# Optimization experiments

Measured on AMD Instinct MI355X. Metric: run time of the kernel, lower is better.

Reference implementation:

```python
import jax, jax.numpy as jnp
import numpy as np

N_FFT = 256
HOP = 64
HS = 126  # window hop in STFT frames (hard-coded in original)


def _stft(x):
    # torch.stft(center=True, pad_mode='reflect', window=None -> rectangular,
    # onesided=True, normalized=False). x: [B, N] -> [B, T, F] (time-major,
    # matching the module's permute(0,1,3,2)).
    pad = N_FFT // 2
    xp = jnp.pad(x, ((0, 0), (pad, pad)), mode='reflect')
    T = x.shape[-1] // HOP + 1
    idx = jnp.arange(T)[:, None] * HOP + jnp.arange(N_FFT)[None, :]  # [T, n_fft]
    frames = xp[:, idx]  # [B, T, n_fft]
    return jnp.fft.rfft(frames, axis=-1)  # [B, T, F=129]


def _spec_match(mix, aux):
    mixS = _stft(mix[:, 0, :])  # [B, Tm, F] complex
    auxS = _stft(aux[:, 0, :])  # [B, Ta, F] complex
    B, Tm, F = mixS.shape
    Ta = auxS.shape[1]
    length = (Ta - Tm) // HS
    pad = HS - (Ta - Tm) % HS
    auxS = jnp.pad(auxS, ((0, 0), (0, pad), (0, 0)))
    # All sliding windows at once: [B, W, Tm, F]
    W = length + 2
    widx = jnp.arange(W)[:, None] * HS + jnp.arange(Tm)[None, :]  # [W, Tm]
    wins = auxS[:, widx, :]  # [B, W, Tm, F]
    # Real part of complex cosine similarity, elementwise
    m = mixS[:, None]  # [B, 1, Tm, F]
    sim = (m.real * wins.real + m.imag * wins.imag) / (jnp.abs(m) * jnp.abs(wins))
    flat = sim.reshape(B, W, -1)
    n = flat.shape[-1]
    # torch.median = lower median; torch.median returns NaN if any NaN present
    srt = jnp.sort(flat, axis=-1)
    med = srt[..., (n - 1) // 2]
    med = jnp.where(jnp.isnan(flat).any(-1), -jnp.inf, med)
    best = jnp.argmax(med, axis=1)  # [B], first max like Python max()
    sel = jnp.take_along_axis(wins, best[:, None, None, None], axis=1)  # [B,1,Tm,F]
    return jnp.concatenate([sel.real, sel.imag], axis=1)  # [B, 2, Tm, F]


def setup_inputs() -> dict:
    key = jax.random.key(0)
    k1, k2 = jax.random.split(key)
    mix = jax.random.normal(k1, (8, 1, 65536), dtype=jnp.float32)
    aux = jax.random.normal(k2, (8, 1, 262144), dtype=jnp.float32)
    return {"mix": mix, "aux": aux}


def reference(mix, aux):
    return _spec_match(mix, aux)
```

## Files before the change

kernel.cpp:

```cpp
#include <hip/hip_runtime.h>
#include <math.h>

constexpr int NFFT  = 256;
constexpr int HOP   = 64;
constexpr int NBIN  = 129;
constexpr int NB    = 8;
constexpr int LMIX  = 65536;
constexpr int LAUX  = 262144;
constexpr int TM    = 1025;
constexpr int TA    = 4097;
constexpr int TROWS = 4175;
constexpr int HS    = 126;
constexpr int W     = 26;
constexpr int NJOBS = NB * W;
constexpr int NVAL  = TM * NBIN;
constexpr int KMED  = (NVAL - 1) / 2;
constexpr int CHUNKS = 8;
constexpr int NBA   = 1024;
constexpr int FPB   = 4;
constexpr int MIXBLKS = (TM + FPB - 1) / FPB;
constexpr int AUXBLKS = (TROWS + FPB - 1) / FPB;

constexpr size_t MIXN_OFF  = 0;
constexpr size_t MIXN_BYTES = (size_t)NB * TM * NBIN * sizeof(float2);
constexpr size_t AUXN_OFF  = MIXN_OFF + MIXN_BYTES;
constexpr size_t AUXN_BYTES = (size_t)NB * TROWS * NBIN * sizeof(float2);
constexpr size_t HIST_OFF  = AUXN_OFF + AUXN_BYTES;
constexpr size_t HIST_BYTES = (size_t)NJOBS * CHUNKS * NBA * 4;
constexpr size_t CAND_OFF  = HIST_OFF + HIST_BYTES;
constexpr size_t CAND_BYTES = (size_t)NJOBS * NVAL * 4;
constexpr size_t NAN_OFF   = CAND_OFF + CAND_BYTES;
constexpr size_t NAN_BYTES = (size_t)NJOBS * CHUNKS * 4;
constexpr size_t NCAND_OFF = NAN_OFF + NAN_BYTES;
constexpr size_t KREM_OFF  = NCAND_OFF + 832;
constexpr size_t MED_OFF   = KREM_OFF + 832;

__device__ __forceinline__ float2 twiddle(int k) {
    float s, c;
    sincosf((float)(-2.0 * 3.14159265358979323846 / 256.0) * (float)k, &s, &c);
    return make_float2(c, s);
}

__global__ void stft_all(const float* __restrict__ mix, const float* __restrict__ aux,
                         float2* __restrict__ mixN, float2* __restrict__ auxN,
                         unsigned* __restrict__ ncand)
{
    constexpr int NX = 64 * (FPB - 1) + NFFT;
    __shared__ float  xs[NX];
    __shared__ float2 Y[FPB][16][16];
    __shared__ float2 cis16[16];

    const int tid = threadIdx.x;
    const int b   = blockIdx.y;
    const int bx  = blockIdx.x;
    const bool isMix = bx < MIXBLKS;
    const int f0 = (isMix ? bx : bx - MIXBLKS) * FPB;
    const int L       = isMix ? LMIX : LAUX;
    const int Tframes = isMix ? TM : TA;
    const int Trows   = isMix ? TM : TROWS;
    const float* x    = isMix ? mix : aux;
    float2* out       = isMix ? mixN : auxN;

    if (bx == 0 && b == 0 && tid < NJOBS) ncand[tid] = 0u;

    if (tid < 16) cis16[tid] = twiddle(16 * tid);

    for (int i = tid; i < NX; i += 256) {
        int j = f0 * HOP + i - 128;
        if (j < 0) j = -j;
        if (j >= L) j = 2 * L - 2 - j;
        xs[i] = x[(size_t)b * L + j];
    }
    __syncthreads();

    const int n1 = (tid >> 4) & 15;
    const int r  = tid & 15;
    #pragma unroll
    for (int f = 0; f < FPB; ++f) {
        float re = 0.f, im = 0.f;
        int idx = 0;
        #pragma unroll
        for (int n2 = 0; n2 < 16; ++n2) {
            float  v = xs[f * HOP + n1 + 16 * n2];
            float2 t = cis16[idx];
            re = fmaf(v, t.x, re);
            im = fmaf(v, t.y, im);
            idx = (idx + r) & 15;
        }
        Y[f][n1][r] = make_float2(re, im);
    }
    __syncthreads();

    const float QNAN = __int_as_float(0x7FC00000);
    auto emit = [&](int fr, int k, float ar, float ai) {
        if (fr >= Trows) return;
        float2 o;
        if (fr < Tframes) {
            float inv = rsqrtf(ar * ar + ai * ai);
            o = make_float2(ar * inv, ai * inv);
        } else {
            o = make_float2(QNAN, QNAN);
        }
        out[((size_t)b * Trows + fr) * NBIN + k] = o;
    };

    {
        const int jjA = tid, jjB = tid + 256;
        const int fA = jjA / NBIN, kA = jjA - fA * NBIN;
        const int fB = jjB / NBIN, kB = jjB - fB * NBIN;
        const float2 dkA = twiddle(kA);
        const float2 dkB = twiddle(kB);
        float trA = 1.f, tiA = 0.f, arA = 0.f, aiA = 0.f;
        float trB = 1.f, tiB = 0.f, arB = 0.f, aiB = 0.f;
        #pragma unroll
        for (int s = 0; s < 16; ++s) {
            float2 yA = Y[fA][s][kA & 15];
            float2 yB = Y[fB][s][kB & 15];
            arA = fmaf(trA, yA.x, arA); arA = fmaf(-tiA, yA.y, arA);
            aiA = fmaf(trA, yA.y, aiA); aiA = fmaf( tiA, yA.x, aiA);
            arB = fmaf(trB, yB.x, arB); arB = fmaf(-tiB, yB.y, arB);
            aiB = fmaf(trB, yB.y, aiB); aiB = fmaf( tiB, yB.x, aiB);
            float nrA = trA * dkA.x - tiA * dkA.y;
            tiA = fmaf(trA, dkA.y, tiA * dkA.x); trA = nrA;
            float nrB = trB * dkB.x - tiB * dkB.y;
            tiB = fmaf(trB, dkB.y, tiB * dkB.x); trB = nrB;
        }
        emit(f0 + fA, kA, arA, aiA);
        emit(f0 + fB, kB, arB, aiB);
    }
    if (tid < FPB * NBIN - 512) {
        const int jj = 512 + tid;
        const int f = jj / NBIN, k = jj - f * NBIN;
        const float2 dk = twiddle(k);
        float tr = 1.f, ti = 0.f, ar = 0.f, ai = 0.f;
        #pragma unroll
        for (int s = 0; s < 16; ++s) {
            float2 y = Y[f][s][k & 15];
            ar = fmaf(tr, y.x, ar); ar = fmaf(-ti, y.y, ar);
            ai = fmaf(tr, y.y, ai); ai = fmaf( ti, y.x, ai);
            float nr = tr * dk.x - ti * dk.y;
            ti = fmaf(tr, dk.y, ti * dk.x); tr = nr;
        }
        emit(f0 + f, k, ar, ai);
    }
}

__device__ __forceinline__ unsigned flip_key(float s) {
    unsigned u = __float_as_uint(s);
    return (u & 0x80000000u) ? ~u : (u | 0x80000000u);
}

__device__ __forceinline__ unsigned qbin(float s) {
    if (!(s == s)) return (unsigned)(NBA - 1);
    int bq = (int)floorf(fmaf(s, 512.f, 512.f));
    bq = max(0, min(NBA - 1, bq));
    return (unsigned)bq;
}

template<int PER>
__device__ __forceinline__ void rank_find(const unsigned (&bins)[PER], unsigned target,
                                          unsigned& out_bin, unsigned& out_rem)
{
    __shared__ unsigned wtot[4];
    __shared__ unsigned result[2];
    const int tid  = threadIdx.x;
    const int lane = tid & 63;
    const int wid  = tid >> 6;

    unsigned st = 0;
    #pragma unroll
    for (int i = 0; i < PER; ++i) st += bins[i];

    unsigned inc = st;
    #pragma unroll
    for (int d = 1; d < 64; d <<= 1) {
        unsigned v = __shfl_up(inc, d);
        if (lane >= d) inc += v;
    }
    if (lane == 63) wtot[wid] = inc;
    __syncthreads();

    unsigned wbase = 0;
    for (int wme = 0; wme < wid; ++wme) wbase += wtot[wme];
    unsigned ex = wbase + inc - st;
    if ((ex <= target) && (target < ex + st)) {
        unsigned cum = ex;
        #pragma unroll
        for (int i = 0; i < PER; ++i) {
            if (cum + bins[i] > target) {
                result[0] = (unsigned)(tid * PER + i);
                result[1] = target - cum;
                break;
            }
            cum += bins[i];
        }
    }
    __syncthreads();
    out_bin = result[0];
    out_rem = result[1];
}

__global__ void sim_hist(const float2* __restrict__ mixN, const float2* __restrict__ auxN,
                         unsigned* __restrict__ hist, unsigned* __restrict__ nanCnt)
{
    constexpr int NCOPY   = 4;
    constexpr int HSTRIDE = NBA + 1;
    __shared__ unsigned lh[NCOPY * HSTRIDE];
    __shared__ unsigned bnan;
    const int tid   = threadIdx.x;
    const int chunk = blockIdx.x;
    const int job   = blockIdx.y;
    const int b = job / W;
    const int w = job - b * W;
    unsigned* lhc = lh + ((tid >> 4) & (NCOPY - 1)) * HSTRIDE;

    for (int i = tid; i < NCOPY * HSTRIDE; i += 256) lh[i] = 0;
    if (tid == 0) bnan = 0;
    __syncthreads();

    unsigned localnan = 0;
    const float2* mrow = mixN + (size_t)b * TM * NBIN;
    const float2* arow = auxN + ((size_t)b * TROWS + (size_t)w * HS) * NBIN;

    const int pad = b & 1;
    const int lim = pad + ((NVAL - pad) & ~1);

    for (int i = pad + (chunk * 256 + tid) * 2; i < lim; i += CHUNKS * 512) {
        float4 mv = *reinterpret_cast<const float4*>(mrow + i);
        float4 av = *reinterpret_cast<const float4*>(arow + i);
        float s0 = fmaf(mv.x, av.x, mv.y * av.y);
        float s1 = fmaf(mv.z, av.z, mv.w * av.w);
        if (!(s0 == s0)) localnan++;
        if (!(s1 == s1)) localnan++;
        atomicAdd(&lhc[qbin(s0)], 1u);
        atomicAdd(&lhc[qbin(s1)], 1u);
    }
    if (chunk == 0 && tid == 0) {
        int ie = pad ? 0 : NVAL - 1;
        float2 m = mrow[ie];
        float2 a = arow[ie];
        float s = fmaf(m.x, a.x, m.y * a.y);
        if (!(s == s)) localnan++;
        atomicAdd(&lhc[qbin(s)], 1u);
    }
    if (localnan) atomicAdd(&bnan, localnan);
    __syncthreads();

    unsigned* gh = hist + ((size_t)job * CHUNKS + chunk) * NBA;
    for (int i = tid; i < NBA; i += 256)
        gh[i] = lh[i] + lh[HSTRIDE + i] + lh[2 * HSTRIDE + i] + lh[3 * HSTRIDE + i];
    if (tid == 0) nanCnt[job * CHUNKS + chunk] = bnan;
}

__global__ void sim_compact(const float2* __restrict__ mixN, const float2* __restrict__ auxN,
                            const unsigned* __restrict__ hist, unsigned* __restrict__ cand,
                            unsigned* __restrict__ ncand, unsigned* __restrict__ krem)
{
    const int tid   = threadIdx.x;
    const int chunk = blockIdx.x;
    const int job   = blockIdx.y;
    const int b = job / W;
    const int w = job - b * W;

    unsigned bins[NBA / 256];
    const unsigned* h = hist + (size_t)job * CHUNKS * NBA;
    #pragma unroll
    for (int i = 0; i < NBA / 256; ++i) {
        unsigned v = 0;
        int bin = tid * (NBA / 256) + i;
        #pragma unroll
        for (int c = 0; c < CHUNKS; ++c) v += h[(size_t)c * NBA + bin];
        bins[i] = v;
    }
    unsigned sb, rem;
    rank_find<NBA / 256>(bins, (unsigned)KMED, sb, rem);
    if (chunk == 0 && tid == 0) krem[job] = rem;

    unsigned* candj  = cand + (size_t)job * NVAL;
    unsigned* ncandj = ncand + job;
    const int lane = tid & 63;

    const float2* mrow = mixN + (size_t)b * TM * NBIN;
    const float2* arow = auxN + ((size_t)b * TROWS + (size_t)w * HS) * NBIN;

    const int pad = b & 1;
    const int lim = pad + ((NVAL - pad) & ~1);

    for (int i = pad + (chunk * 256 + tid) * 2; i < lim; i += CHUNKS * 512) {
        float4 mv = *reinterpret_cast<const float4*>(mrow + i);
        float4 av = *reinterpret_cast<const float4*>(arow + i);
        float sv[2];
        sv[0] = fmaf(mv.x, av.x, mv.y * av.y);
        sv[1] = fmaf(mv.z, av.z, mv.w * av.w);
        #pragma unroll
        for (int u = 0; u < 2; ++u) {
            bool pred = (qbin(sv[u]) == sb);
            unsigned long long m = __ballot(pred);
            if (m) {
                int leader = __ffsll(m) - 1;
                unsigned base = 0;
                if (lane == leader) base = atomicAdd(ncandj, (unsigned)__popcll(m));
                base = (unsigned)__shfl((int)base, leader);
                if (pred) candj[base + __popcll(m & ((1ull << lane) - 1ull))] = flip_key(sv[u]);
            }
        }
    }
    if (chunk == 0 && tid == 0) {
        int ie = pad ? 0 : NVAL - 1;
        float2 m = mrow[ie];
        float2 a = arow[ie];
        float s = fmaf(m.x, a.x, m.y * a.y);
        if (qbin(s) == sb) {
            unsigned idx = atomicAdd(ncandj, 1u);
            candj[idx] = flip_key(s);
        }
    }
}

__global__ void select_kernel(const unsigned* __restrict__ cand, const unsigned* __restrict__ ncand,
                              const unsigned* __restrict__ krem, const unsigned* __restrict__ nanCnt,
                              float* __restrict__ med)
{
    __shared__ unsigned h[2048];
    const int job = blockIdx.x;
    const int tid = threadIdx.x;
    const unsigned* c = cand + (size_t)job * NVAL;
    const unsigned n = ncand[job];
    unsigned pref = 0, tgt = krem[job];

    for (int ph = 0; ph < 3; ++ph) {
        for (int i = tid; i < 2048; i += 256) h[i] = 0;
        __syncthreads();
        for (unsigned i = tid; i < n; i += 256) {
            unsigned k = c[i];
            if (ph == 0) atomicAdd(&h[k >> 21], 1u);
            else if (ph == 1) { if ((k >> 21) == (pref >> 21)) atomicAdd(&h[(k >> 10) & 2047u], 1u); }
            else { if ((k >> 10) == (pref >> 10)) atomicAdd(&h[k & 1023u], 1u); }
        }
        __syncthreads();

        unsigned bins[8];
        #pragma unroll
        for (int i = 0; i < 8; ++i) bins[i] = h[tid * 8 + i];
        unsigned sb, rem;
        rank_find<8>(bins, tgt, sb, rem);

        if (ph == 0)      pref = sb << 21;
        else if (ph == 1) pref |= sb << 10;
        else              pref |= sb;
        tgt = rem;
        __syncthreads();
    }

    if (tid == 0) {
        unsigned nan = 0;
        #pragma unroll
        for (int c2 = 0; c2 < CHUNKS; ++c2) nan += nanCnt[job * CHUNKS + c2];
        unsigned key = pref;
        unsigned u = (key & 0x80000000u) ? (key ^ 0x80000000u) : ~key;
        med[job] = (nan > 0u) ? -INFINITY : __uint_as_float(u);
    }
}

__global__ void gather_stft(const float* __restrict__ x, const float* __restrict__ med,
                            float* __restrict__ out)
{
    constexpr int NX = 64 * (FPB - 1) + NFFT;
    __shared__ float  xs[NX];
    __shared__ float2 Y[FPB][16][16];
    __shared__ float2 cis16[16];
    __shared__ int sh_best;

    const int tid = threadIdx.x;
    const int b   = blockIdx.y;
    const int t0  = blockIdx.x * FPB;

    if (tid == 0) {
        float mx = -INFINITY; int bi = 0;
        for (int w = 0; w < W; ++w) {
            float v = med[b * W + w];
            if (v > mx) { mx = v; bi = w; }
        }
        sh_best = bi;
    }
    if (tid < 16) cis16[tid] = twiddle(16 * tid);
    __syncthreads();

    const int fr0 = sh_best * HS + t0;

    for (int i = tid; i < NX; i += 256) {
        int j = fr0 * HOP + i - 128;
        if (j < 0) j = -j;
        if (j >= LAUX) j = 2 * LAUX - 2 - j;
        j = max(0, min(LAUX - 1, j));
        xs[i] = x[(size_t)b * LAUX + j];
    }
    __syncthreads();

    const int n1 = (tid >> 4) & 15;
    const int r  = tid & 15;
    #pragma unroll
    for (int f = 0; f < FPB; ++f) {
        float re = 0.f, im = 0.f;
        int idx = 0;
        #pragma unroll
        for (int n2 = 0; n2 < 16; ++n2) {
            float  v = xs[f * HOP + n1 + 16 * n2];
            float2 t = cis16[idx];
            re = fmaf(v, t.x, re);
            im = fmaf(v, t.y, im);
            idx = (idx + r) & 15;
        }
        Y[f][n1][r] = make_float2(re, im);
    }
    __syncthreads();

    for (int jj = tid; jj < FPB * NBIN; jj += 256) {
        int f  = jj / NBIN;
        int k  = jj - f * NBIN;
        int t  = t0 + f;
        if (t >= TM) continue;
        float ar = 0.f, ai = 0.f;
        if (fr0 + f < TA) {
            float2 dk = twiddle(k);
            float tr = 1.f, ti = 0.f;
            #pragma unroll
            for (int s = 0; s < 16; ++s) {
                float2 y = Y[f][s][k & 15];
                ar = fmaf(tr, y.x, ar); ar = fmaf(-ti, y.y, ar);
                ai = fmaf(tr, y.y, ai); ai = fmaf( ti, y.x, ai);
                float nr = tr * dk.x - ti * dk.y;
                ti = fmaf(tr, dk.y, ti * dk.x);
                tr = nr;
            }
        }
        size_t o = (size_t)t * NBIN + k;
        out[(size_t)(b * 2 + 0) * NVAL + o] = ar;
        out[(size_t)(b * 2 + 1) * NVAL + o] = ai;
    }
}

extern "C" void kernel_launch(void* const* d_in, const int* in_sizes, int n_in,
                              void* d_out, int out_size, void* d_ws, size_t ws_size,
                              hipStream_t stream)
{
    const float* mix = (const float*)d_in[0];
    const float* aux = (const float*)d_in[1];
    float* out = (float*)d_out;
    char* ws = (char*)d_ws;

    float2*   mixN = (float2*)(ws + MIXN_OFF);
    float2*   auxN = (float2*)(ws + AUXN_OFF);
    unsigned* hist = (unsigned*)(ws + HIST_OFF);
    unsigned* cand = (unsigned*)(ws + CAND_OFF);
    unsigned* nanC = (unsigned*)(ws + NAN_OFF);
    unsigned* ncand= (unsigned*)(ws + NCAND_OFF);
    unsigned* krem = (unsigned*)(ws + KREM_OFF);
    float*    med  = (float*)(ws + MED_OFF);

    stft_all<<<dim3(MIXBLKS + AUXBLKS, NB), 256, 0, stream>>>(mix, aux, mixN, auxN, ncand);
    sim_hist<<<dim3(CHUNKS, NJOBS), 256, 0, stream>>>(mixN, auxN, hist, nanC);
    sim_compact<<<dim3(CHUNKS, NJOBS), 256, 0, stream>>>(mixN, auxN, hist, cand, ncand, krem);
    select_kernel<<<NJOBS, 256, 0, stream>>>(cand, ncand, krem, nanC, med);
    gather_stft<<<dim3((TM + FPB - 1) / FPB, NB), 256, 0, stream>>>(aux, med, out);
}
```

Before: 136.5 us.

## Materialize similarity keys once and replace recompute-compaction with in-shared candidate select

The similarity pass now writes every flipped-float key to a workspace buffer while building the histogram. A small scan kernel then picks the median bin, and the select kernel compacts matching keys from that buffer into shared memory before the radix refinement. This replaces the second read of mixN/auxN with its global atomic compaction. The STFT kernels also use a 256-entry shared twiddle table in place of recursive twiddle multiplication, and loop over frames inside the n2 loop. The cost is writing and re-reading about 110 MB of keys, and a fallback full scan if a bin holds more than SEL_CAP entries.

```diff
diff --git a/kernel.cpp b/kernel.cpp
--- a/kernel.cpp
+++ b/kernel.cpp
@@ -14,41 +14,36 @@
 constexpr int W     = 26;
 constexpr int NJOBS = NB * W;
 constexpr int NVAL  = TM * NBIN;
+constexpr int NVALP = 132228;
 constexpr int KMED  = (NVAL - 1) / 2;
 constexpr int CHUNKS = 8;
 constexpr int NBA   = 1024;
 constexpr int FPB   = 4;
 constexpr int MIXBLKS = (TM + FPB - 1) / FPB;
 constexpr int AUXBLKS = (TROWS + FPB - 1) / FPB;
+constexpr int SEL_CAP = 12288;
 
 constexpr size_t MIXN_OFF  = 0;
 constexpr size_t MIXN_BYTES = (size_t)NB * TM * NBIN * sizeof(float2);
 constexpr size_t AUXN_OFF  = MIXN_OFF + MIXN_BYTES;
 constexpr size_t AUXN_BYTES = (size_t)NB * TROWS * NBIN * sizeof(float2);
-constexpr size_t HIST_OFF  = AUXN_OFF + AUXN_BYTES;
+constexpr size_t KEYS_OFF  = AUXN_OFF + AUXN_BYTES;
+constexpr size_t KEYS_BYTES = (size_t)NJOBS * NVALP * 4;
+constexpr size_t HIST_OFF  = KEYS_OFF + KEYS_BYTES;
 constexpr size_t HIST_BYTES = (size_t)NJOBS * CHUNKS * NBA * 4;
-constexpr size_t CAND_OFF  = HIST_OFF + HIST_BYTES;
-constexpr size_t CAND_BYTES = (size_t)NJOBS * NVAL * 4;
-constexpr size_t NAN_OFF   = CAND_OFF + CAND_BYTES;
+constexpr size_t NAN_OFF   = HIST_OFF + HIST_BYTES;
 constexpr size_t NAN_BYTES = (size_t)NJOBS * CHUNKS * 4;
-constexpr size_t NCAND_OFF = NAN_OFF + NAN_BYTES;
-constexpr size_t KREM_OFF  = NCAND_OFF + 832;
+constexpr size_t SELBIN_OFF= NAN_OFF + NAN_BYTES;
+constexpr size_t KREM_OFF  = SELBIN_OFF + 832;
 constexpr size_t MED_OFF   = KREM_OFF + 832;
 
-__device__ __forceinline__ float2 twiddle(int k) {
-    float s, c;
-    sincosf((float)(-2.0 * 3.14159265358979323846 / 256.0) * (float)k, &s, &c);
-    return make_float2(c, s);
-}
-
 __global__ void stft_all(const float* __restrict__ mix, const float* __restrict__ aux,
-                         float2* __restrict__ mixN, float2* __restrict__ auxN,
-                         unsigned* __restrict__ ncand)
+                         float2* __restrict__ mixN, float2* __restrict__ auxN)
 {
     constexpr int NX = 64 * (FPB - 1) + NFFT;
     __shared__ float  xs[NX];
-    __shared__ float2 Y[FPB][16][16];
-    __shared__ float2 cis16[16];
+    __shared__ float2 Yl[FPB][16][16];
+    __shared__ float2 tw[256];
 
     const int tid = threadIdx.x;
     const int b   = blockIdx.y;
@@ -61,9 +56,8 @@
     const float* x    = isMix ? mix : aux;
     float2* out       = isMix ? mixN : auxN;
 
-    if (bx == 0 && b == 0 && tid < NJOBS) ncand[tid] = 0u;
-
-    if (tid < 16) cis16[tid] = twiddle(16 * tid);
+    { float sv, cv; sincosf((float)(-2.0 * 3.14159265358979323846 / 256.0) * (float)tid, &sv, &cv);
+      tw[tid] = make_float2(cv, sv); }
 
     for (int i = tid; i < NX; i += 256) {
         int j = f0 * HOP + i - 128;
@@ -75,20 +69,26 @@
 
     const int n1 = (tid >> 4) & 15;
     const int r  = tid & 15;
-    #pragma unroll
-    for (int f = 0; f < FPB; ++f) {
-        float re = 0.f, im = 0.f;
+    float reA[FPB], imA[FPB];
+    #pragma unroll
+    for (int f = 0; f < FPB; ++f) { reA[f] = 0.f; imA[f] = 0.f; }
+    {
         int idx = 0;
+        const int step = (r * 16) & 255;
         #pragma unroll
         for (int n2 = 0; n2 < 16; ++n2) {
-            float  v = xs[f * HOP + n1 + 16 * n2];
-            float2 t = cis16[idx];
-            re = fmaf(v, t.x, re);
-            im = fmaf(v, t.y, im);
-            idx = (idx + r) & 15;
-        }
-        Y[f][n1][r] = make_float2(re, im);
-    }
+            float2 t = tw[idx];
+            #pragma unroll
+            for (int f = 0; f < FPB; ++f) {
+                float v = xs[f * HOP + n1 + 16 * n2];
+                reA[f] = fmaf(v, t.x, reA[f]);
+                imA[f] = fmaf(v, t.y, imA[f]);
+            }
+            idx = (idx + step) & 255;
+        }
+    }
+    #pragma unroll
+    for (int f = 0; f < FPB; ++f) Yl[f][n1][r] = make_float2(reA[f], imA[f]);
     __syncthreads();
 
     const float QNAN = __int_as_float(0x7FC00000);
@@ -108,22 +108,17 @@
         const int jjA = tid, jjB = tid + 256;
         const int fA = jjA / NBIN, kA = jjA - fA * NBIN;
         const int fB = jjB / NBIN, kB = jjB - fB * NBIN;
-        const float2 dkA = twiddle(kA);
-        const float2 dkB = twiddle(kB);
-        float trA = 1.f, tiA = 0.f, arA = 0.f, aiA = 0.f;
-        float trB = 1.f, tiB = 0.f, arB = 0.f, aiB = 0.f;
+        float arA = 0.f, aiA = 0.f, arB = 0.f, aiB = 0.f;
+        int ia = 0, ib = 0;
         #pragma unroll
         for (int s = 0; s < 16; ++s) {
-            float2 yA = Y[fA][s][kA & 15];
-            float2 yB = Y[fB][s][kB & 15];
-            arA = fmaf(trA, yA.x, arA); arA = fmaf(-tiA, yA.y, arA);
-            aiA = fmaf(trA, yA.y, aiA); aiA = fmaf( tiA, yA.x, aiA);
-            arB = fmaf(trB, yB.x, arB); arB = fmaf(-tiB, yB.y, arB);
-            aiB = fmaf(trB, yB.y, aiB); aiB = fmaf( tiB, yB.x, aiB);
-            float nrA = trA * dkA.x - tiA * dkA.y;
-            tiA = fmaf(trA, dkA.y, tiA * dkA.x); trA = nrA;
-            float nrB = trB * dkB.x - tiB * dkB.y;
-            tiB = fmaf(trB, dkB.y, tiB * dkB.x); trB = nrB;
+            float2 tA = tw[ia], tB = tw[ib];
+            float2 yA = Yl[fA][s][kA & 15], yB = Yl[fB][s][kB & 15];
+            arA = fmaf(tA.x, yA.x, arA); arA = fmaf(-tA.y, yA.y, arA);
+            aiA = fmaf(tA.x, yA.y, aiA); aiA = fmaf( tA.y, yA.x, aiA);
+            arB = fmaf(tB.x, yB.x, arB); arB = fmaf(-tB.y, yB.y, arB);
+            aiB = fmaf(tB.x, yB.y, aiB); aiB = fmaf( tB.y, yB.x, aiB);
+            ia = (ia + kA) & 255; ib = (ib + kB) & 255;
         }
         emit(f0 + fA, kA, arA, aiA);
         emit(f0 + fB, kB, arB, aiB);
@@ -131,15 +126,15 @@
     if (tid < FPB * NBIN - 512) {
         const int jj = 512 + tid;
         const int f = jj / NBIN, k = jj - f * NBIN;
-        const float2 dk = twiddle(k);
-        float tr = 1.f, ti = 0.f, ar = 0.f, ai = 0.f;
+        float ar = 0.f, ai = 0.f;
+        int ia = 0;
         #pragma unroll
         for (int s = 0; s < 16; ++s) {
-            float2 y = Y[f][s][k & 15];
-            ar = fmaf(tr, y.x, ar); ar = fmaf(-ti, y.y, ar);
-            ai = fmaf(tr, y.y, ai); ai = fmaf( ti, y.x, ai);
-            float nr = tr * dk.x - ti * dk.y;
-            ti = fmaf(tr, dk.y, ti * dk.x); tr = nr;
+            float2 t = tw[ia];
+            float2 y = Yl[f][s][k & 15];
+            ar = fmaf(t.x, y.x, ar); ar = fmaf(-t.y, y.y, ar);
+            ai = fmaf(t.x, y.y, ai); ai = fmaf( t.y, y.x, ai);
+            ia = (ia + k) & 255;
         }
         emit(f0 + f, k, ar, ai);
     }
@@ -149,7 +144,10 @@
     unsigned u = __float_as_uint(s);
     return (u & 0x80000000u) ? ~u : (u | 0x80000000u);
 }
-
+__device__ __forceinline__ float unflip_key(unsigned k) {
+    unsigned u = (k & 0x80000000u) ? (k ^ 0x80000000u) : ~k;
+    return __uint_as_float(u);
+}
 __device__ __forceinline__ unsigned qbin(float s) {
     if (!(s == s)) return (unsigned)(NBA - 1);
     int bq = (int)floorf(fmaf(s, 512.f, 512.f));
@@ -200,8 +198,9 @@
     out_rem = result[1];
 }
 
-__global__ void sim_hist(const float2* __restrict__ mixN, const float2* __restrict__ auxN,
-                         unsigned* __restrict__ hist, unsigned* __restrict__ nanCnt)
+__global__ void sim_keys(const float2* __restrict__ mixN, const float2* __restrict__ auxN,
+                         unsigned* __restrict__ keys, unsigned* __restrict__ hist,
+                         unsigned* __restrict__ nanCnt)
 {
     constexpr int NCOPY   = 4;
     constexpr int HSTRIDE = NBA + 1;
@@ -221,6 +220,7 @@
     unsigned localnan = 0;
     const float2* mrow = mixN + (size_t)b * TM * NBIN;
     const float2* arow = auxN + ((size_t)b * TROWS + (size_t)w * HS) * NBIN;
+    unsigned* kj = keys + (size_t)job * NVALP;
 
     const int pad = b & 1;
     const int lim = pad + ((NVAL - pad) & ~1);
@@ -234,6 +234,7 @@
         if (!(s1 == s1)) localnan++;
         atomicAdd(&lhc[qbin(s0)], 1u);
         atomicAdd(&lhc[qbin(s1)], 1u);
+        *reinterpret_cast<uint2*>(kj + i) = make_uint2(flip_key(s0), flip_key(s1));
     }
     if (chunk == 0 && tid == 0) {
         int ie = pad ? 0 : NVAL - 1;
@@ -242,6 +243,7 @@
         float s = fmaf(m.x, a.x, m.y * a.y);
         if (!(s == s)) localnan++;
         atomicAdd(&lhc[qbin(s)], 1u);
+        kj[ie] = flip_key(s);
     }
     if (localnan) atomicAdd(&bnan, localnan);
     __syncthreads();
@@ -252,102 +254,99 @@
     if (tid == 0) nanCnt[job * CHUNKS + chunk] = bnan;
 }
 
-__global__ void sim_compact(const float2* __restrict__ mixN, const float2* __restrict__ auxN,
-                            const unsigned* __restrict__ hist, unsigned* __restrict__ cand,
-                            unsigned* __restrict__ ncand, unsigned* __restrict__ krem)
-{
-    const int tid   = threadIdx.x;
-    const int chunk = blockIdx.x;
-    const int job   = blockIdx.y;
-    const int b = job / W;
-    const int w = job - b * W;
-
-    unsigned bins[NBA / 256];
+__global__ void scan_bins(const unsigned* __restrict__ hist, unsigned* __restrict__ selbin,
+                          unsigned* __restrict__ krem)
+{
+    constexpr int PER = NBA / 256;
+    const int tid = threadIdx.x;
+    const int job = blockIdx.x;
     const unsigned* h = hist + (size_t)job * CHUNKS * NBA;
-    #pragma unroll
-    for (int i = 0; i < NBA / 256; ++i) {
+
+    unsigned bins[PER];
+    #pragma unroll
+    for (int i = 0; i < PER; ++i) {
         unsigned v = 0;
-        int bin = tid * (NBA / 256) + i;
+        int bin = tid * PER + i;
         #pragma unroll
         for (int c = 0; c < CHUNKS; ++c) v += h[(size_t)c * NBA + bin];
         bins[i] = v;
     }
     unsigned sb, rem;
-    rank_find<NBA / 256>(bins, (unsigned)KMED, sb, rem);
-    if (chunk == 0 && tid == 0) krem[job] = rem;
-
-    unsigned* candj  = cand + (size_t)job * NVAL;
-    unsigned* ncandj = ncand + job;
-    const int lane = tid & 63;
-
-    const float2* mrow = mixN + (size_t)b * TM * NBIN;
-    const float2* arow = auxN + ((size_t)b * TROWS + (size_t)w * HS) * NBIN;
-
-    const int pad = b & 1;
-    const int lim = pad + ((NVAL - pad) & ~1);
-
-    for (int i = pad + (chunk * 256 + tid) * 2; i < lim; i += CHUNKS * 512) {
-        float4 mv = *reinterpret_cast<const float4*>(mrow + i);
-        float4 av = *reinterpret_cast<const float4*>(arow + i);
-        float sv[2];
-        sv[0] = fmaf(mv.x, av.x, mv.y * av.y);
-        sv[1] = fmaf(mv.z, av.z, mv.w * av.w);
-        #pragma unroll
-        for (int u = 0; u < 2; ++u) {
-            bool pred = (qbin(sv[u]) == sb);
-            unsigned long long m = __ballot(pred);
-            if (m) {
-                int leader = __ffsll(m) - 1;
-                unsigned base = 0;
-                if (lane == leader) base = atomicAdd(ncandj, (unsigned)__popcll(m));
-                base = (unsigned)__shfl((int)base, leader);
-                if (pred) candj[base + __popcll(m & ((1ull << lane) - 1ull))] = flip_key(sv[u]);
-            }
-        }
-    }
-    if (chunk == 0 && tid == 0) {
-        int ie = pad ? 0 : NVAL - 1;
-        float2 m = mrow[ie];
-        float2 a = arow[ie];
-        float s = fmaf(m.x, a.x, m.y * a.y);
-        if (qbin(s) == sb) {
-            unsigned idx = atomicAdd(ncandj, 1u);
-            candj[idx] = flip_key(s);
-        }
-    }
-}
-
-__global__ void select_kernel(const unsigned* __restrict__ cand, const unsigned* __restrict__ ncand,
+    rank_find<PER>(bins, (unsigned)KMED, sb, rem);
+    if (tid == 0) { selbin[job] = sb; krem[job] = rem; }
+}
+
+__global__ void select_kernel(const unsigned* __restrict__ keys, const unsigned* __restrict__ selbin,
                               const unsigned* __restrict__ krem, const unsigned* __restrict__ nanCnt,
                               float* __restrict__ med)
 {
+    __shared__ unsigned ck[SEL_CAP];
     __shared__ unsigned h[2048];
+    __shared__ unsigned nov;
     const int job = blockIdx.x;
     const int tid = threadIdx.x;
-    const unsigned* c = cand + (size_t)job * NVAL;
-    const unsigned n = ncand[job];
+    const unsigned* kj = keys + (size_t)job * NVALP;
+    const unsigned sb = selbin[job];
+
+    if (tid == 0) nov = 0;
+    __syncthreads();
+
+    const uint4* k4 = reinterpret_cast<const uint4*>(kj);
+    const int n4 = NVAL / 4;
+    for (int i = tid; i < n4; i += 256) {
+        uint4 v = k4[i];
+        unsigned kk[4] = { v.x, v.y, v.z, v.w };
+        #pragma unroll
+        for (int u = 0; u < 4; ++u) {
+            if (qbin(unflip_key(kk[u])) == sb) {
+                unsigned p = atomicAdd(&nov, 1u);
+                if (p < SEL_CAP) ck[p] = kk[u];
+            }
+        }
+    }
+    if (tid == 0) {
+        unsigned kk = kj[NVAL - 1];
+        if (qbin(unflip_key(kk)) == sb) {
+            unsigned p = atomicAdd(&nov, 1u);
+            if (p < SEL_CAP) ck[p] = kk;
+        }
+    }
+    __syncthreads();
+
+    const unsigned n = nov;
+    const bool fits = (n <= (unsigned)SEL_CAP);
     unsigned pref = 0, tgt = krem[job];
 
     for (int ph = 0; ph < 3; ++ph) {
         for (int i = tid; i < 2048; i += 256) h[i] = 0;
         __syncthreads();
-        for (unsigned i = tid; i < n; i += 256) {
-            unsigned k = c[i];
-            if (ph == 0) atomicAdd(&h[k >> 21], 1u);
-            else if (ph == 1) { if ((k >> 21) == (pref >> 21)) atomicAdd(&h[(k >> 10) & 2047u], 1u); }
-            else { if ((k >> 10) == (pref >> 10)) atomicAdd(&h[k & 1023u], 1u); }
+        if (fits) {
+            for (unsigned i = tid; i < n; i += 256) {
+                unsigned k = ck[i];
+                if (ph == 0) atomicAdd(&h[k >> 21], 1u);
+                else if (ph == 1) { if ((k >> 21) == (pref >> 21)) atomicAdd(&h[(k >> 10) & 2047u], 1u); }
+                else { if ((k >> 10) == (pref >> 10)) atomicAdd(&h[k & 1023u], 1u); }
+            }
+        } else {
+            for (int i = tid; i < NVAL; i += 256) {
+                unsigned k = kj[i];
+                if (qbin(unflip_key(k)) != sb) continue;
+                if (ph == 0) atomicAdd(&h[k >> 21], 1u);
+                else if (ph == 1) { if ((k >> 21) == (pref >> 21)) atomicAdd(&h[(k >> 10) & 2047u], 1u); }
+                else { if ((k >> 10) == (pref >> 10)) atomicAdd(&h[k & 1023u], 1u); }
+            }
         }
         __syncthreads();
 
         unsigned bins[8];
         #pragma unroll
         for (int i = 0; i < 8; ++i) bins[i] = h[tid * 8 + i];
-        unsigned sb, rem;
-        rank_find<8>(bins, tgt, sb, rem);
-
-        if (ph == 0)      pref = sb << 21;
-        else if (ph == 1) pref |= sb << 10;
-        else              pref |= sb;
+        unsigned sb2, rem;
+        rank_find<8>(bins, tgt, sb2, rem);
+
+        if (ph == 0)      pref = sb2 << 21;
+        else if (ph == 1) pref |= sb2 << 10;
+        else              pref |= sb2;
         tgt = rem;
         __syncthreads();
     }
@@ -355,10 +354,8 @@
     if (tid == 0) {
         unsigned nan = 0;
         #pragma unroll
-        for (int c2 = 0; c2 < CHUNKS; ++c2) nan += nanCnt[job * CHUNKS + c2];
-        unsigned key = pref;
-        unsigned u = (key & 0x80000000u) ? (key ^ 0x80000000u) : ~key;
-        med[job] = (nan > 0u) ? -INFINITY : __uint_as_float(u);
+        for (int c = 0; c < CHUNKS; ++c) nan += nanCnt[job * CHUNKS + c];
+        med[job] = (nan > 0u) ? -INFINITY : unflip_key(pref);
     }
 }
 
@@ -367,8 +364,8 @@
 {
     constexpr int NX = 64 * (FPB - 1) + NFFT;
     __shared__ float  xs[NX];
-    __shared__ float2 Y[FPB][16][16];
-    __shared__ float2 cis16[16];
+    __shared__ float2 Yl[FPB][16][16];
+    __shared__ float2 tw[256];
     __shared__ int sh_best;
 
     const int tid = threadIdx.x;
@@ -383,7 +380,8 @@
         }
         sh_best = bi;
     }
-    if (tid < 16) cis16[tid] = twiddle(16 * tid);
+    { float sv, cv; sincosf((float)(-2.0 * 3.14159265358979323846 / 256.0) * (float)tid, &sv, &cv);
+      tw[tid] = make_float2(cv, sv); }
     __syncthreads();
 
     const int fr0 = sh_best * HS + t0;
@@ -399,20 +397,26 @@
 
     const int n1 = (tid >> 4) & 15;
     const int r  = tid & 15;
-    #pragma unroll
-    for (int f = 0; f < FPB; ++f) {
-        float re = 0.f, im = 0.f;
+    float reA[FPB], imA[FPB];
+    #pragma unroll
+    for (int f = 0; f < FPB; ++f) { reA[f] = 0.f; imA[f] = 0.f; }
+    {
         int idx = 0;
+        const int step = (r * 16) & 255;
         #pragma unroll
         for (int n2 = 0; n2 < 16; ++n2) {
-            float  v = xs[f * HOP + n1 + 16 * n2];
-            float2 t = cis16[idx];
-            re = fmaf(v, t.x, re);
-            im = fmaf(v, t.y, im);
-            idx = (idx + r) & 15;
-        }
-        Y[f][n1][r] = make_float2(re, im);
-    }
+            float2 t = tw[idx];
+            #pragma unroll
+            for (int f = 0; f < FPB; ++f) {
+                float v = xs[f * HOP + n1 + 16 * n2];
+                reA[f] = fmaf(v, t.x, reA[f]);
+                imA[f] = fmaf(v, t.y, imA[f]);
+            }
+            idx = (idx + step) & 255;
+        }
+    }
+    #pragma unroll
+    for (int f = 0; f < FPB; ++f) Yl[f][n1][r] = make_float2(reA[f], imA[f]);
     __syncthreads();
 
     for (int jj = tid; jj < FPB * NBIN; jj += 256) {
@@ -422,16 +426,14 @@
         if (t >= TM) continue;
         float ar = 0.f, ai = 0.f;
         if (fr0 + f < TA) {
-            float2 dk = twiddle(k);
-            float tr = 1.f, ti = 0.f;
+            int ia = 0;
             #pragma unroll
             for (int s = 0; s < 16; ++s) {
-                float2 y = Y[f][s][k & 15];
-                ar = fmaf(tr, y.x, ar); ar = fmaf(-ti, y.y, ar);
-                ai = fmaf(tr, y.y, ai); ai = fmaf( ti, y.x, ai);
-                float nr = tr * dk.x - ti * dk.y;
-                ti = fmaf(tr, dk.y, ti * dk.x);
-                tr = nr;
+                float2 tv = tw[ia];
+                float2 y = Yl[f][s][k & 15];
+                ar = fmaf(tv.x, y.x, ar); ar = fmaf(-tv.y, y.y, ar);
+                ai = fmaf(tv.x, y.y, ai); ai = fmaf( tv.y, y.x, ai);
+                ia = (ia + k) & 255;
             }
         }
         size_t o = (size_t)t * NBIN + k;
@@ -451,16 +453,16 @@
 
     float2*   mixN = (float2*)(ws + MIXN_OFF);
     float2*   auxN = (float2*)(ws + AUXN_OFF);
+    unsigned* keys = (unsigned*)(ws + KEYS_OFF);
     unsigned* hist = (unsigned*)(ws + HIST_OFF);
-    unsigned* cand = (unsigned*)(ws + CAND_OFF);
     unsigned* nanC = (unsigned*)(ws + NAN_OFF);
-    unsigned* ncand= (unsigned*)(ws + NCAND_OFF);
+    unsigned* selb = (unsigned*)(ws + SELBIN_OFF);
     unsigned* krem = (unsigned*)(ws + KREM_OFF);
     float*    med  = (float*)(ws + MED_OFF);
 
-    stft_all<<<dim3(MIXBLKS + AUXBLKS, NB), 256, 0, stream>>>(mix, aux, mixN, auxN, ncand);
-    sim_hist<<<dim3(CHUNKS, NJOBS), 256, 0, stream>>>(mixN, auxN, hist, nanC);
-    sim_compact<<<dim3(CHUNKS, NJOBS), 256, 0, stream>>>(mixN, auxN, hist, cand, ncand, krem);
-    select_kernel<<<NJOBS, 256, 0, stream>>>(cand, ncand, krem, nanC, med);
-    gather_stft<<<dim3((TM + FPB - 1) / FPB, NB), 256, 0, stream>>>(aux, med, out);
-}
+    stft_all<<<dim3(MIXBLKS + AUXBLKS, NB), 256, 0, stream>>>(mix, aux, mixN, auxN);
+    sim_keys<<<dim3(CHUNKS, NJOBS), 256, 0, stream>>>(mixN, auxN, keys, hist, nanC);
+    scan_bins<<<NJOBS, 256, 0, stream>>>(hist, selb, krem);
+    select_kernel<<<NJOBS, 256, 0, stream>>>(keys, selb, krem, nanC, med);
+    gather_stft<<<dim3(MIXBLKS, NB), 256, 0, stream>>>(aux, med, out);
+}
```

Result: slower. 195.1 us (+43.0%).

## Swizzle workgroup IDs across batches and widen STFT frames per block

Applied to the files above, without the earlier changes.

Flattens every grid to 1D and decodes the block index so that the batch index is the fastest-varying component. The likely aim is to spread consecutive workgroups over XCDs and memory channels. The STFT kernel now handles 8 frames per block instead of 4, with the first-stage DFT loop interchanged so each twiddle load serves all frames. Per-bin twiddles come from a shared 256-entry table rather than sincosf in each thread. Larger blocks mean fewer workgroups and more registers per thread, which may reduce occupancy.

```diff
diff --git a/kernel.cpp b/kernel.cpp
--- a/kernel.cpp
+++ b/kernel.cpp
@@ -17,9 +17,11 @@
 constexpr int KMED  = (NVAL - 1) / 2;
 constexpr int CHUNKS = 8;
 constexpr int NBA   = 1024;
-constexpr int FPB   = 4;
+constexpr int FPB   = 8;
 constexpr int MIXBLKS = (TM + FPB - 1) / FPB;
 constexpr int AUXBLKS = (TROWS + FPB - 1) / FPB;
+constexpr int GFPB  = 4;
+constexpr int GBLKS = (TM + GFPB - 1) / GFPB;
 
 constexpr size_t MIXN_OFF  = 0;
 constexpr size_t MIXN_BYTES = (size_t)NB * TM * NBIN * sizeof(float2);
@@ -35,9 +37,11 @@
 constexpr size_t KREM_OFF  = NCAND_OFF + 832;
 constexpr size_t MED_OFF   = KREM_OFF + 832;
 
+constexpr float TWOPI_N = (float)(-2.0 * 3.14159265358979323846 / 256.0);
+
 __device__ __forceinline__ float2 twiddle(int k) {
     float s, c;
-    sincosf((float)(-2.0 * 3.14159265358979323846 / 256.0) * (float)k, &s, &c);
+    sincosf(TWOPI_N * (float)k, &s, &c);
     return make_float2(c, s);
 }
 
@@ -47,22 +51,25 @@
 {
     constexpr int NX = 64 * (FPB - 1) + NFFT;
     __shared__ float  xs[NX];
-    __shared__ float2 Y[FPB][16][16];
+    __shared__ float2 Yl[FPB][16][16];
+    __shared__ float2 tw256[256];
     __shared__ float2 cis16[16];
 
-    const int tid = threadIdx.x;
-    const int b   = blockIdx.y;
-    const int bx  = blockIdx.x;
-    const bool isMix = bx < MIXBLKS;
-    const int f0 = (isMix ? bx : bx - MIXBLKS) * FPB;
+    const int tid  = threadIdx.x;
+    const int wgid = blockIdx.x;
+    const int b    = wgid & 7;
+    const int t    = wgid >> 3;
+    const bool isMix = t < MIXBLKS;
+    const int f0 = (isMix ? t : t - MIXBLKS) * FPB;
     const int L       = isMix ? LMIX : LAUX;
     const int Tframes = isMix ? TM : TA;
     const int Trows   = isMix ? TM : TROWS;
     const float* x    = isMix ? mix : aux;
     float2* out       = isMix ? mixN : auxN;
 
-    if (bx == 0 && b == 0 && tid < NJOBS) ncand[tid] = 0u;
-
+    if (wgid == 0 && tid < NJOBS) ncand[tid] = 0u;
+
+    tw256[tid] = twiddle(tid);
     if (tid < 16) cis16[tid] = twiddle(16 * tid);
 
     for (int i = tid; i < NX; i += 256) {
@@ -75,19 +82,24 @@
 
     const int n1 = (tid >> 4) & 15;
     const int r  = tid & 15;
-    #pragma unroll
-    for (int f = 0; f < FPB; ++f) {
-        float re = 0.f, im = 0.f;
+    {
+        float reA[FPB], imA[FPB];
+        #pragma unroll
+        for (int f = 0; f < FPB; ++f) { reA[f] = 0.f; imA[f] = 0.f; }
         int idx = 0;
         #pragma unroll
         for (int n2 = 0; n2 < 16; ++n2) {
-            float  v = xs[f * HOP + n1 + 16 * n2];
-            float2 t = cis16[idx];
-            re = fmaf(v, t.x, re);
-            im = fmaf(v, t.y, im);
+            float2 tv = cis16[idx];
+            #pragma unroll
+            for (int f = 0; f < FPB; ++f) {
+                float v = xs[f * HOP + n1 + 16 * n2];
+                reA[f] = fmaf(v, tv.x, reA[f]);
+                imA[f] = fmaf(v, tv.y, imA[f]);
+            }
             idx = (idx + r) & 15;
         }
-        Y[f][n1][r] = make_float2(re, im);
+        #pragma unroll
+        for (int f = 0; f < FPB; ++f) Yl[f][n1][r] = make_float2(reA[f], imA[f]);
     }
     __syncthreads();
 
@@ -105,37 +117,39 @@
     };
 
     {
-        const int jjA = tid, jjB = tid + 256;
-        const int fA = jjA / NBIN, kA = jjA - fA * NBIN;
-        const int fB = jjB / NBIN, kB = jjB - fB * NBIN;
-        const float2 dkA = twiddle(kA);
-        const float2 dkB = twiddle(kB);
-        float trA = 1.f, tiA = 0.f, arA = 0.f, aiA = 0.f;
-        float trB = 1.f, tiB = 0.f, arB = 0.f, aiB = 0.f;
+        int fc[4], kc[4];
+        float tr[4], ti[4], ar[4], ai[4];
+        float2 dk[4];
+        #pragma unroll
+        for (int c = 0; c < 4; ++c) {
+            int jj = tid + 256 * c;
+            fc[c] = jj / NBIN; kc[c] = jj - fc[c] * NBIN;
+            dk[c] = tw256[kc[c]];
+            tr[c] = 1.f; ti[c] = 0.f; ar[c] = 0.f; ai[c] = 0.f;
+        }
         #pragma unroll
         for (int s = 0; s < 16; ++s) {
-            float2 yA = Y[fA][s][kA & 15];
-            float2 yB = Y[fB][s][kB & 15];
-            arA = fmaf(trA, yA.x, arA); arA = fmaf(-tiA, yA.y, arA);
-            aiA = fmaf(trA, yA.y, aiA); aiA = fmaf( tiA, yA.x, aiA);
-            arB = fmaf(trB, yB.x, arB); arB = fmaf(-tiB, yB.y, arB);
-            aiB = fmaf(trB, yB.y, aiB); aiB = fmaf( tiB, yB.x, aiB);
-            float nrA = trA * dkA.x - tiA * dkA.y;
-            tiA = fmaf(trA, dkA.y, tiA * dkA.x); trA = nrA;
-            float nrB = trB * dkB.x - tiB * dkB.y;
-            tiB = fmaf(trB, dkB.y, tiB * dkB.x); trB = nrB;
-        }
-        emit(f0 + fA, kA, arA, aiA);
-        emit(f0 + fB, kB, arB, aiB);
-    }
-    if (tid < FPB * NBIN - 512) {
-        const int jj = 512 + tid;
+            #pragma unroll
+            for (int c = 0; c < 4; ++c) {
+                float2 y = Yl[fc[c]][s][kc[c] & 15];
+                ar[c] = fmaf(tr[c], y.x, ar[c]); ar[c] = fmaf(-ti[c], y.y, ar[c]);
+                ai[c] = fmaf(tr[c], y.y, ai[c]); ai[c] = fmaf( ti[c], y.x, ai[c]);
+                float nr = tr[c] * dk[c].x - ti[c] * dk[c].y;
+                ti[c] = fmaf(tr[c], dk[c].y, ti[c] * dk[c].x);
+                tr[c] = nr;
+            }
+        }
+        #pragma unroll
+        for (int c = 0; c < 4; ++c) emit(f0 + fc[c], kc[c], ar[c], ai[c]);
+    }
+    if (tid < FPB * NBIN - 1024) {
+        const int jj = 1024 + tid;
         const int f = jj / NBIN, k = jj - f * NBIN;
-        const float2 dk = twiddle(k);
+        const float2 dk = tw256[k];
         float tr = 1.f, ti = 0.f, ar = 0.f, ai = 0.f;
         #pragma unroll
         for (int s = 0; s < 16; ++s) {
-            float2 y = Y[f][s][k & 15];
+            float2 y = Yl[f][s][k & 15];
             ar = fmaf(tr, y.x, ar); ar = fmaf(-ti, y.y, ar);
             ai = fmaf(tr, y.y, ai); ai = fmaf( ti, y.x, ai);
             float nr = tr * dk.x - ti * dk.y;
@@ -149,7 +163,6 @@
     unsigned u = __float_as_uint(s);
     return (u & 0x80000000u) ? ~u : (u | 0x80000000u);
 }
-
 __device__ __forceinline__ unsigned qbin(float s) {
     if (!(s == s)) return (unsigned)(NBA - 1);
     int bq = (int)floorf(fmaf(s, 512.f, 512.f));
@@ -208,10 +221,12 @@
     __shared__ unsigned lh[NCOPY * HSTRIDE];
     __shared__ unsigned bnan;
     const int tid   = threadIdx.x;
-    const int chunk = blockIdx.x;
-    const int job   = blockIdx.y;
-    const int b = job / W;
-    const int w = job - b * W;
+    const int wgid  = blockIdx.x;
+    const int b     = wgid & 7;
+    const int rest  = wgid >> 3;
+    const int w     = rest / CHUNKS;
+    const int chunk = rest - w * CHUNKS;
+    const int job   = b * W + w;
     unsigned* lhc = lh + ((tid >> 4) & (NCOPY - 1)) * HSTRIDE;
 
     for (int i = tid; i < NCOPY * HSTRIDE; i += 256) lh[i] = 0;
@@ -257,10 +272,12 @@
                             unsigned* __restrict__ ncand, unsigned* __restrict__ krem)
 {
     const int tid   = threadIdx.x;
-    const int chunk = blockIdx.x;
-    const int job   = blockIdx.y;
-    const int b = job / W;
-    const int w = job - b * W;
+    const int wgid  = blockIdx.x;
+    const int b     = wgid & 7;
+    const int rest  = wgid >> 3;
+    const int w     = rest / CHUNKS;
+    const int chunk = rest - w * CHUNKS;
+    const int job   = b * W + w;
 
     unsigned bins[NBA / 256];
     const unsigned* h = hist + (size_t)job * CHUNKS * NBA;
@@ -322,8 +339,9 @@
                               float* __restrict__ med)
 {
     __shared__ unsigned h[2048];
-    const int job = blockIdx.x;
-    const int tid = threadIdx.x;
+    const int wgid = blockIdx.x;
+    const int job  = (wgid & 7) * W + (wgid >> 3);
+    const int tid  = threadIdx.x;
     const unsigned* c = cand + (size_t)job * NVAL;
     const unsigned n = ncand[job];
     unsigned pref = 0, tgt = krem[job];
@@ -365,15 +383,17 @@
 __global__ void gather_stft(const float* __restrict__ x, const float* __restrict__ med,
                             float* __restrict__ out)
 {
-    constexpr int NX = 64 * (FPB - 1) + NFFT;
+    constexpr int NX = 64 * (GFPB - 1) + NFFT;
     __shared__ float  xs[NX];
-    __shared__ float2 Y[FPB][16][16];
+    __shared__ float2 Yl[GFPB][16][16];
+    __shared__ float2 tw256[256];
     __shared__ float2 cis16[16];
     __shared__ int sh_best;
 
-    const int tid = threadIdx.x;
-    const int b   = blockIdx.y;
-    const int t0  = blockIdx.x * FPB;
+    const int tid  = threadIdx.x;
+    const int wgid = blockIdx.x;
+    const int b    = wgid & 7;
+    const int t0   = (wgid >> 3) * GFPB;
 
     if (tid == 0) {
         float mx = -INFINITY; int bi = 0;
@@ -383,6 +403,7 @@
         }
         sh_best = bi;
     }
+    tw256[tid] = twiddle(tid);
     if (tid < 16) cis16[tid] = twiddle(16 * tid);
     __syncthreads();
 
@@ -399,45 +420,51 @@
 
     const int n1 = (tid >> 4) & 15;
     const int r  = tid & 15;
-    #pragma unroll
-    for (int f = 0; f < FPB; ++f) {
-        float re = 0.f, im = 0.f;
+    {
+        float reA[GFPB], imA[GFPB];
+        #pragma unroll
+        for (int f = 0; f < GFPB; ++f) { reA[f] = 0.f; imA[f] = 0.f; }
         int idx = 0;
         #pragma unroll
         for (int n2 = 0; n2 < 16; ++n2) {
-            float  v = xs[f * HOP + n1 + 16 * n2];
-            float2 t = cis16[idx];
-            re = fmaf(v, t.x, re);
-            im = fmaf(v, t.y, im);
+            float2 tv = cis16[idx];
+            #pragma unroll
+            for (int f = 0; f < GFPB; ++f) {
+                float v = xs[f * HOP + n1 + 16 * n2];
+                reA[f] = fmaf(v, tv.x, reA[f]);
+                imA[f] = fmaf(v, tv.y, imA[f]);
+            }
             idx = (idx + r) & 15;
         }
-        Y[f][n1][r] = make_float2(re, im);
-    }
-    __syncthreads();
-
-    for (int jj = tid; jj < FPB * NBIN; jj += 256) {
-        int f  = jj / NBIN;
-        int k  = jj - f * NBIN;
-        int t  = t0 + f;
-        if (t >= TM) continue;
+        #pragma unroll
+        for (int f = 0; f < GFPB; ++f) Yl[f][n1][r] = make_float2(reA[f], imA[f]);
+    }
+    __syncthreads();
+
+    auto dotask = [&](int jj) {
+        const int f = jj / NBIN, k = jj - f * NBIN;
+        const int tt = t0 + f;
+        if (tt >= TM) return;
         float ar = 0.f, ai = 0.f;
         if (fr0 + f < TA) {
-            float2 dk = twiddle(k);
+            const float2 dk = tw256[k];
             float tr = 1.f, ti = 0.f;
             #pragma unroll
             for (int s = 0; s < 16; ++s) {
-                float2 y = Y[f][s][k & 15];
+                float2 y = Yl[f][s][k & 15];
                 ar = fmaf(tr, y.x, ar); ar = fmaf(-ti, y.y, ar);
                 ai = fmaf(tr, y.y, ai); ai = fmaf( ti, y.x, ai);
                 float nr = tr * dk.x - ti * dk.y;
-                ti = fmaf(tr, dk.y, ti * dk.x);
-                tr = nr;
-            }
-        }
-        size_t o = (size_t)t * NBIN + k;
+                ti = fmaf(tr, dk.y, ti * dk.x); tr = nr;
+            }
+        }
+        size_t o = (size_t)tt * NBIN + k;
         out[(size_t)(b * 2 + 0) * NVAL + o] = ar;
         out[(size_t)(b * 2 + 1) * NVAL + o] = ai;
-    }
+    };
+    dotask(tid);
+    dotask(tid + 256);
+    if (tid < GFPB * NBIN - 512) dotask(512 + tid);
 }
 
 extern "C" void kernel_launch(void* const* d_in, const int* in_sizes, int n_in,
@@ -458,9 +485,9 @@
     unsigned* krem = (unsigned*)(ws + KREM_OFF);
     float*    med  = (float*)(ws + MED_OFF);
 
-    stft_all<<<dim3(MIXBLKS + AUXBLKS, NB), 256, 0, stream>>>(mix, aux, mixN, auxN, ncand);
-    sim_hist<<<dim3(CHUNKS, NJOBS), 256, 0, stream>>>(mixN, auxN, hist, nanC);
-    sim_compact<<<dim3(CHUNKS, NJOBS), 256, 0, stream>>>(mixN, auxN, hist, cand, ncand, krem);
+    stft_all<<<(MIXBLKS + AUXBLKS) * NB, 256, 0, stream>>>(mix, aux, mixN, auxN, ncand);
+    sim_hist<<<NJOBS * CHUNKS, 256, 0, stream>>>(mixN, auxN, hist, nanC);
+    sim_compact<<<NJOBS * CHUNKS, 256, 0, stream>>>(mixN, auxN, hist, cand, ncand, krem);
     select_kernel<<<NJOBS, 256, 0, stream>>>(cand, ncand, krem, nanC, med);
-    gather_stft<<<dim3((TM + FPB - 1) / FPB, NB), 256, 0, stream>>>(aux, med, out);
-}
+    gather_stft<<<GBLKS * NB, 256, 0, stream>>>(aux, med, out);
+}
```

Result: slower. 179.5 us (+31.5%).
